# Optimization experiments

Measured on AMD Instinct MI355X. Metric: run time of the kernel, lower is better.

The kernel has to match this reference:

```python
import jax, jax.numpy as jnp
import numpy as np
import math

PHI = (1 + math.sqrt(5)) / 2
PI = math.pi
B, L, D, V, NL, PAD = 2, 384, 256, 32000, 3, 0


def _ln(t, eps):
    mu = t.mean(-1, keepdims=True)
    var = ((t - mu) ** 2).mean(-1, keepdims=True)
    return (t - mu) / jnp.sqrt(var + eps)


def setup_inputs() -> dict:
    key = jax.random.key(0)
    ks = jax.random.split(key, 8)
    return {
        'x': jax.random.randint(ks[0], (B, L), 0, V, dtype=jnp.int32),
        'emb_real': jax.random.normal(ks[1], (V, D), jnp.float32) * 0.02,
        'emb_imag': jax.random.normal(ks[2], (V, D), jnp.float32) * 0.02,
        'layer_phases': jax.random.normal(ks[3], (NL, D), jnp.float32) * 0.02,
        'interference_weights': jax.random.normal(ks[4], (NL, D), jnp.float32) * 0.02,
        'energy_levels': jnp.linspace(0.0, 1.0, D).astype(jnp.float32),
        'excitation_factor': jnp.ones((1,), jnp.float32) * 0.1,
        'phase_preservation': jnp.ones((NL, D), jnp.float32) * 0.1,
        'coherence_factor': jnp.ones((NL, 1), jnp.float32) * 0.1,
        'W_attn': jax.random.normal(ks[5], (NL, D, D), jnp.float32) * 0.02,
        'out_w': jax.random.normal(ks[6], (2 * D, V), jnp.float32) * 0.02,
        'out_b': jnp.zeros((V,), jnp.float32),
    }


def _forward(x, emb_real, emb_imag, layer_phases, interference_weights,
             energy_levels, excitation_factor, phase_preservation,
             coherence_factor, W_attn, out_w, out_b):
    re = emb_real[x] * 0.1                      # [B,L,D]
    _unused_imag = emb_imag[x] * 0.1            # imag embedding unused downstream (as in original)
    # ---- EnhancedDynamicPhaseSpace ----
    fr = jnp.zeros_like(re)
    fi = jnp.zeros_like(re)
    for i in range(NL):
        pa = jnp.tanh(layer_phases[i]) * PI * PHI      # [D]
        r = _ln(re * jnp.cos(pa), 1e-8)
        im = _ln(re * jnp.sin(pa), 1e-8)
        w = jnp.tanh(interference_weights[i])
        r = r * w
        im = im * w
        a = 2.0 * PI * i / NL
        ca, sa = math.cos(a), math.sin(a)
        fr = fr + r * ca - im * sa
        fi = fi + r * sa + im * ca
    amp = jnp.sqrt(fr * fr + fi * fi + 1e-8)
    coll = (amp < 0.1).astype(re.dtype)
    exc = jnp.exp(energy_levels) * excitation_factor   # [D]
    fr = fr + coll * exc
    fi = fi + coll * exc
    nrm = jnp.sqrt(fr * fr + fi * fi + 1e-8)
    real = jnp.clip(fr / nrm, -1.0, 1.0)
    imag = jnp.clip(fi / nrm, -1.0, 1.0)
    # ---- 3 QuantumStatePreservingAttention layers ----
    pad_mask = (x == PAD)                               # [B,L]
    scale = D ** (-0.5)
    for i in range(NL):
        # q/k/v LayerNorms are parameter-free here and q=k=v, so one norm each
        nr = _ln(real, 1e-5)
        ni = _ln(imag, 1e-5)
        ph = jnp.arctan2(ni + 1e-8, nr + 1e-8)          # [B,L,D]
        pdiff = ph[:, :, None, :] - ph[:, None, :, :]   # [B,L,L,D]
        interf = jnp.cos(pdiff)                         # [B,L,L,D]
        # mean over last dim of (interf @ W) == interf . row-means of W (same math)
        w_mean = W_attn[i].mean(axis=1)                 # [D]
        scores = jnp.einsum('blmd,d->blm', interf, w_mean) * scale
        scores = jnp.where(pad_mask[:, None, :], -jnp.inf, scores)
        attn = jnp.clip(jax.nn.softmax(scores, axis=-1), 1e-6, 1.0)
        out_r = jnp.einsum('blm,bmd->bld', attn, nr)
        out_i = jnp.einsum('blm,bmd->bld', attn, ni)
        coh = interf.mean(axis=(-1, -2))                # [B,L]
        cf = jax.nn.sigmoid(coherence_factor[i]) * coh[..., None]
        phase = jnp.arctan2(out_i + 1e-8, out_r + 1e-8)
        pres = jax.nn.sigmoid(phase_preservation[i]) * cf
        pr = out_r * jnp.cos(phase * pres)
        pim = out_i * jnp.sin(phase * pres)
        real = jnp.clip(_ln(real + 0.01 * pr, 1e-8), -1.0, 1.0)
        _dead = _ln(imag + 0.01 * pim, 1e-8)            # computed then overwritten in original
        imag = real                                     # original bug: imag = clamp(real, -1, 1)
    combined = _ln(jnp.concatenate([real, imag], axis=-1), 1e-5)
    logits = jnp.clip((combined @ out_w + out_b) * 0.1, -10.0, 10.0)
    return logits


def reference(x, emb_real, emb_imag, layer_phases, interference_weights,
              energy_levels, excitation_factor, phase_preservation,
              coherence_factor, W_attn, out_w, out_b):
    return _forward(x, emb_real, emb_imag, layer_phases, interference_weights,
                    energy_levels, excitation_factor, phase_preservation,
                    coherence_factor, W_attn, out_w, out_b)
```

## Files before the change

kernel.cpp:

```cpp
#include <hip/hip_runtime.h>
#include <hip/hip_bf16.h>
#include <math.h>

typedef __hip_bfloat16 bf16;
typedef __bf16 bf16x8 __attribute__((ext_vector_type(8)));
typedef float f32x4 __attribute__((ext_vector_type(4)));

#define NTOK 768
#define SEQ  384
#define DDIM 256
#define VOC  32000

__device__ __forceinline__ float bf2f(bf16 v) { return __bfloat162float(v); }

__device__ __forceinline__ bool probe_bf(const void* energy) {
    return ((const unsigned short*)energy)[1] != 0;
}
__device__ __forceinline__ float ldin(const void* p, long i, bool bf) {
    return bf ? bf2f(((const bf16*)p)[i]) : ((const float*)p)[i];
}

__device__ __forceinline__ float blk_sum256s(float v, float* red) {
    #pragma unroll
    for (int o = 32; o > 0; o >>= 1) v += __shfl_down(v, o, 64);
    __syncthreads();
    if ((threadIdx.x & 63) == 0) red[threadIdx.x >> 6] = v;
    __syncthreads();
    return red[0] + red[1] + red[2] + red[3];
}

__device__ __forceinline__ void np_emit(int t, int d, float nrv, float niv, bool dual,
                                        const float* __restrict__ wm,
                                        float* __restrict__ nrO, float* __restrict__ niO,
                                        float* __restrict__ Co, float* __restrict__ So,
                                        bf16* __restrict__ ASh, bf16* __restrict__ ASl,
                                        bf16* __restrict__ BSh, bf16* __restrict__ BSl)
{
    float ph = atan2f(niv + 1e-8f, nrv + 1e-8f);
    float Cv = cosf(ph), Sv = sinf(ph);
    long idx = (long)t * DDIM + d;
    nrO[idx] = nrv;
    if (dual) niO[idx] = niv;
    Co[idx] = Cv;
    So[idx] = Sv;
    float wv = wm[d];
    float aC = Cv * wv, aS = Sv * wv;
    long o0 = (long)t * 512 + d, o1 = o0 + 256;
    bf16 h;
    h = __float2bfloat16(aC); ASh[o0] = h; ASl[o0] = __float2bfloat16(aC - bf2f(h));
    h = __float2bfloat16(aS); ASh[o1] = h; ASl[o1] = __float2bfloat16(aS - bf2f(h));
    h = __float2bfloat16(Cv); BSh[o0] = h; BSl[o0] = __float2bfloat16(Cv - bf2f(h));
    h = __float2bfloat16(Sv); BSh[o1] = h; BSl[o1] = __float2bfloat16(Sv - bf2f(h));
}

__device__ __forceinline__ void gload_lds16(const bf16* g, bf16* l) {
    __builtin_amdgcn_global_load_lds(
        (const __attribute__((address_space(1))) unsigned int*)g,
        (__attribute__((address_space(3))) unsigned int*)l,
        16, 0, 0);
}


__device__ __forceinline__ void scores_unit(int l0, int m0, int b, char* smem,
    const bf16* __restrict__ ASh, const bf16* __restrict__ ASl,
    const bf16* __restrict__ BSh, const bf16* __restrict__ BSl,
    float* __restrict__ scores)
{
    bf16* ldsA0 = (bf16*)smem;
    bf16* ldsA1 = ldsA0 + 2048;
    bf16* ldsB0 = ldsA1 + 2048;
    bf16* ldsB1 = ldsB0 + 2048;
    int tid = threadIdx.x, lane = tid & 63, wid = tid >> 6;
    int wr = wid >> 1, wc = wid & 1;
    int lrow = lane >> 3, cbs = (lane & 7) ^ lrow;
    const bf16* src = (wid == 0 ? ASh : wid == 1 ? ASl : wid == 2 ? BSh : BSl)
                      + (size_t)(b * SEQ + (wid < 2 ? l0 : m0)) * 512;
    bf16* ld = (wid == 0 ? ldsA0 : wid == 1 ? ldsA1 : wid == 2 ? ldsB0 : ldsB1);
    f32x4 acc = {};
    for (int k0 = 0; k0 < 512; k0 += 64) {
        #pragma unroll
        for (int q = 0; q < 4; ++q)
            gload_lds16(src + (size_t)(q * 8 + lrow) * 512 + k0 + cbs * 8, ld + q * 512);
        __syncthreads();
        #pragma unroll
        for (int ks = 0; ks < 2; ++ks) {
            int cb = ks * 64 + (lane >> 4) * 16;
            int rowb = wc * 16 + (lane & 15);
            int offb = rowb * 128 + (cb ^ ((rowb & 7) << 4));
            bf16x8 bh = *(const bf16x8*)((const char*)ldsB0 + offb);
            bf16x8 bl = *(const bf16x8*)((const char*)ldsB1 + offb);
            int rowa = wr * 16 + (lane & 15);
            int offa = rowa * 128 + (cb ^ ((rowa & 7) << 4));
            bf16x8 ah = *(const bf16x8*)((const char*)ldsA0 + offa);
            bf16x8 al = *(const bf16x8*)((const char*)ldsA1 + offa);
            acc = __builtin_amdgcn_mfma_f32_16x16x32_bf16(ah, bh, acc, 0, 0, 0);
            acc = __builtin_amdgcn_mfma_f32_16x16x32_bf16(ah, bl, acc, 0, 0, 0);
            acc = __builtin_amdgcn_mfma_f32_16x16x32_bf16(al, bh, acc, 0, 0, 0);
        }
        __syncthreads();
    }
    int mm = m0 + wc * 16 + (lane & 15);
    int lbase = l0 + wr * 16 + (lane >> 4) * 4;
    #pragma unroll
    for (int i = 0; i < 4; ++i)
        scores[(size_t)(b * SEQ + lbase + i) * SEQ + mm] = acc[i];
}

__device__ __forceinline__ void transpose_unit(int m0, int d0, int b, char* smem, int dual,
    const float* __restrict__ nr, const float* __restrict__ ni,
    bf16* __restrict__ nrTh, bf16* __restrict__ nrTl,
    bf16* __restrict__ niTh, bf16* __restrict__ niTl)
{
    float* tr = (float*)smem;
    float* ti = tr + 64 * 65;
    int c = threadIdx.x & 63, rr = threadIdx.x >> 6;
    #pragma unroll
    for (int i = 0; i < 16; ++i) {
        int r = i * 4 + rr;
        tr[r * 65 + c] = nr[(b * SEQ + m0 + r) * DDIM + d0 + c];
        if (dual) ti[r * 65 + c] = ni[(b * SEQ + m0 + r) * DDIM + d0 + c];
    }
    __syncthreads();
    #pragma unroll
    for (int i = 0; i < 16; ++i) {
        int dd = i * 4 + rr;
        long o = (long)(b * DDIM + d0 + dd) * SEQ + m0 + c;
        float vr = tr[c * 65 + dd];
        bf16 h;
        h = __float2bfloat16(vr); nrTh[o] = h; nrTl[o] = __float2bfloat16(vr - bf2f(h));
        if (dual) {
            float vi = ti[c * 65 + dd];
            h = __float2bfloat16(vi); niTh[o] = h; niTl[o] = __float2bfloat16(vi - bf2f(h));
        }
    }
}

__device__ __forceinline__ void sums_unit(int c, int b,
    const float* __restrict__ C, const float* __restrict__ S,
    float* __restrict__ Cp, float* __restrict__ Sp)
{
    int d = threadIdx.x;
    float cs = 0.f, ss = 0.f;
    int base = (b * SEQ + c * 16) * DDIM + d;
    #pragma unroll
    for (int m = 0; m < 16; ++m) { cs += C[base + m * DDIM]; ss += S[base + m * DDIM]; }
    Cp[(b * 24 + c) * DDIM + d] = cs;
    Sp[(b * 24 + c) * DDIM + d] = ss;
}

__global__ __launch_bounds__(256)
void phaseA_k(const bf16* __restrict__ ASh, const bf16* __restrict__ ASl,
              const bf16* __restrict__ BSh, const bf16* __restrict__ BSl,
              float* __restrict__ attn,
              const float* __restrict__ nr, const float* __restrict__ ni,
              bf16* __restrict__ nrTh, bf16* __restrict__ nrTl,
              bf16* __restrict__ niTh, bf16* __restrict__ niTl,
              const float* __restrict__ Cc, const float* __restrict__ Ss,
              float* __restrict__ Cp, float* __restrict__ Sp, int dual)
{
    __shared__ __align__(16) char smem[33280];
    int u = blockIdx.x;
    if (u < 288) {
        scores_unit((u % 12) * 32, ((u / 12) % 12) * 32, u / 144, smem,
                    ASh, ASl, BSh, BSl, attn);
    } else if (u < 336) {
        int v = u - 288;
        transpose_unit((v % 6) * 64, ((v / 6) % 4) * 64, v / 24, smem, dual,
                       nr, ni, nrTh, nrTl, niTh, niTl);
    } else {
        int w = u - 336;
        sums_unit(w % 24, w / 24, Cc, Ss, Cp, Sp);
    }
}

__global__ __launch_bounds__(256)
void outfused_k(const float* __restrict__ scores, const int* __restrict__ x,
                const bf16* __restrict__ nrTh, const bf16* __restrict__ nrTl,
                const bf16* __restrict__ niTh, const bf16* __restrict__ niTl,
                float* __restrict__ outr, float* __restrict__ outi, int dual)
{
    __shared__ __align__(16) char PhL[32 * 768];
    __shared__ __align__(16) char PlL[32 * 768];
    __shared__ __align__(16) char Bb[8192];
    int l0 = blockIdx.x * 32, d0 = blockIdx.y * 32, b = blockIdx.z;
    int tid = threadIdx.x, lane = tid & 63, wid = tid >> 6;

    int msk = 0;
    #pragma unroll
    for (int j = 0; j < 6; ++j)
        if (x[b * SEQ + lane + j * 64] == 0) msk |= (1 << j);

    #pragma unroll
    for (int r8 = 0; r8 < 8; ++r8) {
        int r = wid * 8 + r8;
        const float* srow = scores + (size_t)(b * SEQ + l0 + r) * SEQ;
        float v[6];
        float mx = -__builtin_inff();
        #pragma unroll
        for (int j = 0; j < 6; ++j) {
            float s = srow[lane + j * 64];
            if (msk & (1 << j)) s = -__builtin_inff();
            v[j] = s;
            mx = fmaxf(mx, s);
        }
        #pragma unroll
        for (int o = 32; o > 0; o >>= 1) mx = fmaxf(mx, __shfl_xor(mx, o, 64));
        float e[6], sum = 0.f;
        #pragma unroll
        for (int j = 0; j < 6; ++j) { e[j] = expf(v[j] - mx); sum += e[j]; }
        #pragma unroll
        for (int o = 32; o > 0; o >>= 1) sum += __shfl_xor(sum, o, 64);
        #pragma unroll
        for (int j = 0; j < 6; ++j) {
            float p = fminf(fmaxf(e[j] / sum, 1e-6f), 1.0f);
            bf16 h = __float2bfloat16(p);
            bf16 l = __float2bfloat16(p - bf2f(h));
            int c2 = (lane + j * 64) * 2;
            int swz = ((c2 & ~15) ^ ((r & 7) << 4)) | (c2 & 15);
            *(bf16*)(PhL + r * 768 + swz) = h;
            *(bf16*)(PlL + r * 768 + swz) = l;
        }
    }
    __syncthreads();

    int wr = wid >> 1, wc = wid & 1;
    int lrow = lane >> 3, cbs = (lane & 7) ^ lrow;
    int half = wid >> 1;
    int npass = dual ? 2 : 1;

    for (int pass = 0; pass < npass; ++pass) {
        const bf16* srcB = ((wid & 1) ? (pass ? niTl : nrTl) : (pass ? niTh : nrTh))
                           + (size_t)(b * DDIM + d0) * SEQ;
        bf16* ldB = (bf16*)(Bb + (wid & 1) * 4096 + half * 2048);
        f32x4 acc = {};
        for (int k0 = 0; k0 < SEQ; k0 += 64) {
            #pragma unroll
            for (int q = 0; q < 2; ++q)
                gload_lds16(srcB + (size_t)(half * 16 + q * 8 + lrow) * SEQ + k0 + cbs * 8,
                            ldB + q * 512);
            __syncthreads();
            #pragma unroll
            for (int ks = 0; ks < 2; ++ks) {
                int cbk = ks * 64 + (lane >> 4) * 16;
                int rowb = wc * 16 + (lane & 15);
                int offb = rowb * 128 + (cbk ^ ((rowb & 7) << 4));
                bf16x8 bh = *(const bf16x8*)(Bb + offb);
                bf16x8 bl = *(const bf16x8*)(Bb + 4096 + offb);
                int rowa = wr * 16 + (lane & 15);
                int cba = k0 * 2 + cbk;
                int offa = rowa * 768 + (cba ^ ((rowa & 7) << 4));
                bf16x8 ah = *(const bf16x8*)(PhL + offa);
                bf16x8 al = *(const bf16x8*)(PlL + offa);
                acc = __builtin_amdgcn_mfma_f32_16x16x32_bf16(ah, bh, acc, 0, 0, 0);
                acc = __builtin_amdgcn_mfma_f32_16x16x32_bf16(ah, bl, acc, 0, 0, 0);
                acc = __builtin_amdgcn_mfma_f32_16x16x32_bf16(al, bh, acc, 0, 0, 0);
            }
            __syncthreads();
        }
        float* dst = pass ? outi : outr;
        int d = d0 + wc * 16 + (lane & 15);
        int lb = l0 + wr * 16 + (lane >> 4) * 4;
        #pragma unroll
        for (int i = 0; i < 4; ++i)
            dst[(size_t)(b * SEQ + lb + i) * DDIM + d] = acc[i];
    }
}

__global__ __launch_bounds__(256)
void update_k(float* __restrict__ realA,
              const float* __restrict__ outr, const float* __restrict__ outi,
              const float* __restrict__ C, const float* __restrict__ S,
              const float* __restrict__ Cp, const float* __restrict__ Sp,
              const void* __restrict__ pp, const void* __restrict__ cfac,
              const void* __restrict__ energy, int layer, int mode,
              const float* __restrict__ wmNext,
              float* __restrict__ nrO, float* __restrict__ Co, float* __restrict__ So,
              bf16* __restrict__ ASh, bf16* __restrict__ ASl,
              bf16* __restrict__ BSh, bf16* __restrict__ BSl,
              bf16* __restrict__ Ah, bf16* __restrict__ Al)
{
    __shared__ float red[4];
    bool bf = probe_bf(energy);
    int t = blockIdx.x, d = threadIdx.x;
    int b = t / SEQ;
    long idx = (long)t * DDIM + d;
    float cs = 0.f, ss = 0.f;
    #pragma unroll
    for (int c = 0; c < 24; ++c) {
        cs += Cp[(b * 24 + c) * DDIM + d];
        ss += Sp[(b * 24 + c) * DDIM + d];
    }
    float dotv = C[idx] * cs + S[idx] * ss;
    float coh = blk_sum256s(dotv, red) * (1.0f / (384.f * 256.f));
    float cf = (1.f / (1.f + expf(-ldin(cfac, layer, bf)))) * coh;
    float orr = outr[idx], oii = outi[idx];
    float phase = atan2f(oii + 1e-8f, orr + 1e-8f);
    float pres = (1.f / (1.f + expf(-ldin(pp, layer * DDIM + d, bf)))) * cf;
    float pr = orr * cosf(phase * pres);
    float v = realA[idx] + 0.01f * pr;
    float mu = blk_sum256s(v, red) * (1.f / 256.f);
    float dv = v - mu;
    float var = blk_sum256s(dv * dv, red) * (1.f / 256.f);
    float nv = dv / sqrtf(var + 1e-8f);
    nv = fminf(fmaxf(nv, -1.f), 1.f);
    realA[idx] = nv;
    float mu2 = blk_sum256s(nv, red) * (1.f / 256.f);
    float dv2 = nv - mu2;
    float var2 = blk_sum256s(dv2 * dv2, red) * (1.f / 256.f);
    float nn = dv2 / sqrtf(var2 + 1e-5f);
    if (mode == 0) {
        np_emit(t, d, nn, nn, false, wmNext, nrO, nullptr, Co, So, ASh, ASl, BSh, BSl);
    } else {
        bf16 h = __float2bfloat16(nn);
        Ah[idx] = h;
        Al[idx] = __float2bfloat16(nn - bf2f(h));
    }
}

__global__ __launch_bounds__(256)
void phase_kernel(const int* __restrict__ x, const void* __restrict__ emb,
                  const void* __restrict__ lph, const void* __restrict__ iw,
                  const void* __restrict__ energy, const void* __restrict__ excf,
                  const float* __restrict__ wm0,
                  float* __restrict__ realO,
                  float* __restrict__ nrO, float* __restrict__ niO,
                  float* __restrict__ Co, float* __restrict__ So,
                  bf16* __restrict__ ASh, bf16* __restrict__ ASl,
                  bf16* __restrict__ BSh, bf16* __restrict__ BSl)
{
    __shared__ float red[4];
    bool bf = probe_bf(energy);
    int t = blockIdx.x, d = threadIdx.x;
    int tok = x[t];
    float re = ldin(emb, (long)tok * DDIM + d, bf) * 0.1f;
    float fr = 0.f, fi = 0.f;
    const float ca[3] = {1.0f, -0.5f, -0.5f};
    const float sa[3] = {0.0f, 0.86602540378443864676f, -0.86602540378443864676f};
    #pragma unroll
    for (int i = 0; i < 3; ++i) {
        float pa = tanhf(ldin(lph, i * DDIM + d, bf)) * 3.14159265358979323846f;
        pa = pa * 1.61803398874989484820f;
        float vr = re * cosf(pa);
        float vi = re * sinf(pa);
        float mu = blk_sum256s(vr, red) * (1.f / 256.f);
        float dv = vr - mu;
        float var = blk_sum256s(dv * dv, red) * (1.f / 256.f);
        float r = dv / sqrtf(var + 1e-8f);
        mu = blk_sum256s(vi, red) * (1.f / 256.f);
        float di = vi - mu;
        var = blk_sum256s(di * di, red) * (1.f / 256.f);
        float im = di / sqrtf(var + 1e-8f);
        float w = tanhf(ldin(iw, i * DDIM + d, bf));
        r *= w; im *= w;
        fr = fr + r * ca[i] - im * sa[i];
        fi = fi + r * sa[i] + im * ca[i];
    }
    float amp = sqrtf(fr * fr + fi * fi + 1e-8f);
    float ex = expf(ldin(energy, d, bf)) * ldin(excf, 0, bf);
    if (amp < 0.1f) { fr += ex; fi += ex; }
    float nrm = sqrtf(fr * fr + fi * fi + 1e-8f);
    float rr = fminf(fmaxf(fr / nrm, -1.f), 1.f);
    float ii = fminf(fmaxf(fi / nrm, -1.f), 1.f);
    realO[t * DDIM + d] = rr;
    float mu = blk_sum256s(rr, red) * (1.f / 256.f);
    float dv = rr - mu;
    float var = blk_sum256s(dv * dv, red) * (1.f / 256.f);
    float nrv = dv / sqrtf(var + 1e-5f);
    mu = blk_sum256s(ii, red) * (1.f / 256.f);
    float di = ii - mu;
    var = blk_sum256s(di * di, red) * (1.f / 256.f);
    float niv = di / sqrtf(var + 1e-5f);
    np_emit(t, d, nrv, niv, true, wm0, nrO, niO, Co, So, ASh, ASl, BSh, BSl);
}

__global__ __launch_bounds__(256)
void prep1_k(const void* __restrict__ W, const void* __restrict__ Wattn,
             const void* __restrict__ energy,
             bf16* __restrict__ Bh, bf16* __restrict__ Bl, float* __restrict__ wmAll)
{
    bool bf = probe_bf(energy);
    int u = blockIdx.x;
    if (u < 2000) {
        __shared__ float tile[64][65];
        int v0 = (u % 500) * 64, d0 = (u / 500) * 64;
        int c = threadIdx.x & 63, rr = threadIdx.x >> 6;
        #pragma unroll
        for (int i = 0; i < 16; ++i) {
            int r = i * 4 + rr;
            long i1 = (long)(d0 + r) * VOC + v0 + c;
            long i2 = (long)(d0 + r + 256) * VOC + v0 + c;
            tile[r][c] = ldin(W, i1, bf) + ldin(W, i2, bf);
        }
        __syncthreads();
        int d = threadIdx.x & 63, vv = threadIdx.x >> 6;
        #pragma unroll
        for (int i = 0; i < 16; ++i) {
            int v = i * 4 + vv;
            float s = tile[d][v];
            bf16 h = __float2bfloat16(s);
            long o = (long)(v0 + v) * DDIM + d0 + d;
            Bh[o] = h;
            Bl[o] = __float2bfloat16(s - __bfloat162float(h));
        }
    } else {
        int row = (u - 2000) * 4 + (threadIdx.x >> 6);
        int lane = threadIdx.x & 63;
        long base = (long)row * DDIM + lane * 4;
        float s = 0.f;
        #pragma unroll
        for (int j = 0; j < 4; ++j) s += ldin(Wattn, base + j, bf);
        #pragma unroll
        for (int o = 32; o > 0; o >>= 1) s += __shfl_down(s, o, 64);
        if (lane == 0) wmAll[row] = s * (1.f / 256.f) * 0.0625f;
    }
}

__global__ __launch_bounds__(512, 4)
void vocab_gemm(const bf16* __restrict__ Ah, const bf16* __restrict__ Al,
                const bf16* __restrict__ Bh, const bf16* __restrict__ Bl,
                const void* __restrict__ bias, const void* __restrict__ energy,
                void* __restrict__ out)
{
    __shared__ bf16 lds[4][128 * 64];
    bool bf = probe_bf(energy);
    int flat = blockIdx.x + blockIdx.y * 6;
    int xcd = flat & 7, bidx = flat >> 3;
    int swz = (xcd < 4) ? xcd * 188 + bidx : 752 + (xcd - 4) * 187 + bidx;
    int m0 = (swz % 6) * 128, n0 = (swz / 6) * 128;
    int tid = threadIdx.x, lane = tid & 63, wid = tid >> 6;
    int wm = wid >> 2, wn = wid & 3;
    int arr = wid >> 1, half = wid & 1;

    const bf16* src;
    if      (arr == 0) src = Ah + (size_t)m0 * DDIM;
    else if (arr == 1) src = Al + (size_t)m0 * DDIM;
    else if (arr == 2) src = Bh + (size_t)n0 * DDIM;
    else               src = Bl + (size_t)n0 * DDIM;
    src += (size_t)half * 64 * DDIM;
    bf16* ldst = &lds[arr][half * 64 * 64];
    int lrow = lane >> 3;
    int cbs  = (lane & 7) ^ lrow;

    f32x4 acc[4][2] = {};

    for (int k0 = 0; k0 < DDIM; k0 += 64) {
        #pragma unroll
        for (int q = 0; q < 8; ++q) {
            const bf16* gp = src + (size_t)(q * 8 + lrow) * DDIM + k0 + cbs * 8;
            gload_lds16(gp, ldst + q * 512);
        }
        __syncthreads();
        #pragma unroll
        for (int ks = 0; ks < 2; ++ks) {
            int cb = ks * 64 + (lane >> 4) * 16;
            bf16x8 bhf[2], blf[2];
            #pragma unroll
            for (int fn = 0; fn < 2; ++fn) {
                int row = wn * 32 + fn * 16 + (lane & 15);
                int off = row * 128 + (cb ^ ((row & 7) << 4));
                bhf[fn] = *(const bf16x8*)((const char*)&lds[2][0] + off);
                blf[fn] = *(const bf16x8*)((const char*)&lds[3][0] + off);
            }
            #pragma unroll
            for (int fm = 0; fm < 4; ++fm) {
                int row = wm * 64 + fm * 16 + (lane & 15);
                int off = row * 128 + (cb ^ ((row & 7) << 4));
                bf16x8 ah = *(const bf16x8*)((const char*)&lds[0][0] + off);
                bf16x8 al = *(const bf16x8*)((const char*)&lds[1][0] + off);
                #pragma unroll
                for (int fn = 0; fn < 2; ++fn) {
                    acc[fm][fn] = __builtin_amdgcn_mfma_f32_16x16x32_bf16(ah, bhf[fn], acc[fm][fn], 0, 0, 0);
                    acc[fm][fn] = __builtin_amdgcn_mfma_f32_16x16x32_bf16(ah, blf[fn], acc[fm][fn], 0, 0, 0);
                    acc[fm][fn] = __builtin_amdgcn_mfma_f32_16x16x32_bf16(al, bhf[fn], acc[fm][fn], 0, 0, 0);
                }
            }
        }
        __syncthreads();
    }

    #pragma unroll
    for (int fn = 0; fn < 2; ++fn) {
        int n = n0 + wn * 32 + fn * 16 + (lane & 15);
        float bv = ldin(bias, n, bf);
        #pragma unroll
        for (int fm = 0; fm < 4; ++fm) {
            int mbase = m0 + wm * 64 + fm * 16 + (lane >> 4) * 4;
            #pragma unroll
            for (int i = 0; i < 4; ++i) {
                float lg = (acc[fm][fn][i] + bv) * 0.1f;
                lg = fminf(fmaxf(lg, -10.f), 10.f);
                size_t idx = (size_t)(mbase + i) * VOC + n;
                if (bf) ((bf16*)out)[idx] = __float2bfloat16(lg);
                else    ((float*)out)[idx] = lg;
            }
        }
    }
}

extern "C" void kernel_launch(void* const* d_in, const int* in_sizes, int n_in,
                              void* d_out, int out_size, void* d_ws, size_t ws_size,
                              hipStream_t stream) {
    (void)in_sizes; (void)n_in; (void)out_size; (void)ws_size;
    const int*  x        = (const int*)d_in[0];
    const void* emb_real = d_in[1];
    const void* lph      = d_in[3];
    const void* iw       = d_in[4];
    const void* energy   = d_in[5];
    const void* excf     = d_in[6];
    const void* pp       = d_in[7];
    const void* cfac     = d_in[8];
    const void* Wattn    = d_in[9];
    const void* out_w    = d_in[10];
    const void* out_b    = d_in[11];

    float* ws = (float*)d_ws;
    const int TD = NTOK * DDIM;
    float* realA = ws;
    float* nr    = realA + TD;
    float* ni    = nr + TD;
    float* Cc    = ni + TD;
    float* Ss    = Cc + TD;
    float* outr  = Ss + TD;
    float* outi  = outr + TD;
    float* attn  = outi + TD;
    float* Cp    = attn + 2 * SEQ * SEQ;
    float* Sp    = Cp + 48 * DDIM;
    float* wmAll = Sp + 48 * DDIM;
    bf16* Ah  = (bf16*)(wmAll + 768);
    bf16* Al  = Ah + (size_t)NTOK * DDIM;
    bf16* Wth = Al + (size_t)NTOK * DDIM;
    bf16* Wtl = Wth + (size_t)VOC * DDIM;
    bf16* ASh = Wtl + (size_t)VOC * DDIM;
    bf16* ASl = ASh + (size_t)NTOK * 512;
    bf16* BSh = ASl + (size_t)NTOK * 512;
    bf16* BSl = BSh + (size_t)NTOK * 512;
    bf16* nrTh = BSl + (size_t)NTOK * 512;
    bf16* nrTl = nrTh + (size_t)NTOK * DDIM;
    bf16* niTh = nrTl + (size_t)NTOK * DDIM;
    bf16* niTl = niTh + (size_t)NTOK * DDIM;

    prep1_k<<<2192, 256, 0, stream>>>(out_w, Wattn, energy, Wth, Wtl, wmAll);
    phase_kernel<<<NTOK, 256, 0, stream>>>(x, emb_real, lph, iw, energy, excf, wmAll,
                                           realA, nr, ni, Cc, Ss, ASh, ASl, BSh, BSl);
    for (int layer = 0; layer < 3; ++layer) {
        int dual = (layer == 0);
        phaseA_k<<<384, 256, 0, stream>>>(ASh, ASl, BSh, BSl, attn, nr, ni,
                                          nrTh, nrTl, niTh, niTl, Cc, Ss, Cp, Sp, dual);
        outfused_k<<<dim3(12, 8, 2), 256, 0, stream>>>(attn, x, nrTh, nrTl, niTh, niTl,
                                                       outr, outi, dual);
        update_k<<<NTOK, 256, 0, stream>>>(realA, outr, dual ? outi : outr, Cc, Ss,
                                           Cp, Sp, pp, cfac, energy, layer,
                                           (layer < 2) ? 0 : 1,
                                           wmAll + (layer + 1 < 3 ? (layer + 1) * DDIM : 0),
                                           nr, Cc, Ss, ASh, ASl, BSh, BSl, Ah, Al);
    }
    vocab_gemm<<<dim3(6, VOC / 128), 512, 0, stream>>>(Ah, Al, Wth, Wtl, out_b, energy, (void*)d_out);
}
```

Measured before the change: 363.7 us.

## Exploit real==imag in later layers to halve score K and double-buffer LDS loads

For layers after the first, the imaginary input equals the real one, so C==S. Those layers now use a single folded cos term with a factor of 2, which halves the score GEMM K dimension from 512 to 256 and drops the sine sums and stores. The score and output GEMM loops also double-buffer their global-to-LDS loads so the next K tile is fetched while MFMAs run. The outfused kernel computes the real and imaginary products in one pass instead of two. In exchange it uses more LDS, and correctness depends on the algebraic identity sin(atan2(n,n)) == cos(atan2(n,n)).

```diff
diff --git a/kernel.cpp b/kernel.cpp
--- a/kernel.cpp
+++ b/kernel.cpp
@@ -29,7 +29,7 @@
     return red[0] + red[1] + red[2] + red[3];
 }
 
-__device__ __forceinline__ void np_emit(int t, int d, float nrv, float niv, bool dual,
+__device__ __forceinline__ void np_emit(int t, int d, float nrv, float niv,
                                         const float* __restrict__ wm,
                                         float* __restrict__ nrO, float* __restrict__ niO,
                                         float* __restrict__ Co, float* __restrict__ So,
@@ -40,7 +40,7 @@
     float Cv = cosf(ph), Sv = sinf(ph);
     long idx = (long)t * DDIM + d;
     nrO[idx] = nrv;
-    if (dual) niO[idx] = niv;
+    niO[idx] = niv;
     Co[idx] = Cv;
     So[idx] = Sv;
     float wv = wm[d];
@@ -61,43 +61,49 @@
 }
 
 
-__device__ __forceinline__ void scores_unit(int l0, int m0, int b, char* smem,
+__device__ __forceinline__ void scores_unit(int l0, int m0, int b, char* smem, int kd,
     const bf16* __restrict__ ASh, const bf16* __restrict__ ASl,
     const bf16* __restrict__ BSh, const bf16* __restrict__ BSl,
     float* __restrict__ scores)
 {
-    bf16* ldsA0 = (bf16*)smem;
-    bf16* ldsA1 = ldsA0 + 2048;
-    bf16* ldsB0 = ldsA1 + 2048;
-    bf16* ldsB1 = ldsB0 + 2048;
     int tid = threadIdx.x, lane = tid & 63, wid = tid >> 6;
     int wr = wid >> 1, wc = wid & 1;
     int lrow = lane >> 3, cbs = (lane & 7) ^ lrow;
     const bf16* src = (wid == 0 ? ASh : wid == 1 ? ASl : wid == 2 ? BSh : BSl)
-                      + (size_t)(b * SEQ + (wid < 2 ? l0 : m0)) * 512;
-    bf16* ld = (wid == 0 ? ldsA0 : wid == 1 ? ldsA1 : wid == 2 ? ldsB0 : ldsB1);
+                      + (size_t)(b * SEQ + (wid < 2 ? l0 : m0)) * kd;
+    bf16* ld0 = (bf16*)(smem + wid * 4096);
+    bf16* ld1 = (bf16*)(smem + 16384 + wid * 4096);
     f32x4 acc = {};
-    for (int k0 = 0; k0 < 512; k0 += 64) {
-        #pragma unroll
-        for (int q = 0; q < 4; ++q)
-            gload_lds16(src + (size_t)(q * 8 + lrow) * 512 + k0 + cbs * 8, ld + q * 512);
-        __syncthreads();
+    #pragma unroll
+    for (int q = 0; q < 4; ++q)
+        gload_lds16(src + (size_t)(q * 8 + lrow) * kd + cbs * 8, ld0 + q * 512);
+    __syncthreads();
+    int cur = 0;
+    for (int k0 = 0; k0 < kd; k0 += 64) {
+        if (k0 + 64 < kd) {
+            bf16* ld = cur ? ld0 : ld1;
+            #pragma unroll
+            for (int q = 0; q < 4; ++q)
+                gload_lds16(src + (size_t)(q * 8 + lrow) * kd + (k0 + 64) + cbs * 8, ld + q * 512);
+        }
+        const char* base = smem + cur * 16384;
         #pragma unroll
         for (int ks = 0; ks < 2; ++ks) {
             int cb = ks * 64 + (lane >> 4) * 16;
             int rowb = wc * 16 + (lane & 15);
             int offb = rowb * 128 + (cb ^ ((rowb & 7) << 4));
-            bf16x8 bh = *(const bf16x8*)((const char*)ldsB0 + offb);
-            bf16x8 bl = *(const bf16x8*)((const char*)ldsB1 + offb);
+            bf16x8 bh = *(const bf16x8*)(base + 8192 + offb);
+            bf16x8 bl = *(const bf16x8*)(base + 12288 + offb);
             int rowa = wr * 16 + (lane & 15);
             int offa = rowa * 128 + (cb ^ ((rowa & 7) << 4));
-            bf16x8 ah = *(const bf16x8*)((const char*)ldsA0 + offa);
-            bf16x8 al = *(const bf16x8*)((const char*)ldsA1 + offa);
+            bf16x8 ah = *(const bf16x8*)(base + offa);
+            bf16x8 al = *(const bf16x8*)(base + 4096 + offa);
             acc = __builtin_amdgcn_mfma_f32_16x16x32_bf16(ah, bh, acc, 0, 0, 0);
             acc = __builtin_amdgcn_mfma_f32_16x16x32_bf16(ah, bl, acc, 0, 0, 0);
             acc = __builtin_amdgcn_mfma_f32_16x16x32_bf16(al, bh, acc, 0, 0, 0);
         }
         __syncthreads();
+        cur ^= 1;
     }
     int mm = m0 + wc * 16 + (lane & 15);
     int lbase = l0 + wr * 16 + (lane >> 4) * 4;
@@ -135,7 +141,7 @@
     }
 }
 
-__device__ __forceinline__ void sums_unit(int c, int b,
+__device__ __forceinline__ void sums_unit(int c, int b, int dual,
     const float* __restrict__ C, const float* __restrict__ S,
     float* __restrict__ Cp, float* __restrict__ Sp)
 {
@@ -143,9 +149,12 @@
     float cs = 0.f, ss = 0.f;
     int base = (b * SEQ + c * 16) * DDIM + d;
     #pragma unroll
-    for (int m = 0; m < 16; ++m) { cs += C[base + m * DDIM]; ss += S[base + m * DDIM]; }
+    for (int m = 0; m < 16; ++m) {
+        cs += C[base + m * DDIM];
+        if (dual) ss += S[base + m * DDIM];
+    }
     Cp[(b * 24 + c) * DDIM + d] = cs;
-    Sp[(b * 24 + c) * DDIM + d] = ss;
+    if (dual) Sp[(b * 24 + c) * DDIM + d] = ss;
 }
 
 __global__ __launch_bounds__(256)
@@ -156,12 +165,12 @@
               bf16* __restrict__ nrTh, bf16* __restrict__ nrTl,
               bf16* __restrict__ niTh, bf16* __restrict__ niTl,
               const float* __restrict__ Cc, const float* __restrict__ Ss,
-              float* __restrict__ Cp, float* __restrict__ Sp, int dual)
+              float* __restrict__ Cp, float* __restrict__ Sp, int dual, int kd)
 {
     __shared__ __align__(16) char smem[33280];
     int u = blockIdx.x;
     if (u < 288) {
-        scores_unit((u % 12) * 32, ((u / 12) % 12) * 32, u / 144, smem,
+        scores_unit((u % 12) * 32, ((u / 12) % 12) * 32, u / 144, smem, kd,
                     ASh, ASl, BSh, BSl, attn);
     } else if (u < 336) {
         int v = u - 288;
@@ -169,7 +178,7 @@
                        nr, ni, nrTh, nrTl, niTh, niTl);
     } else {
         int w = u - 336;
-        sums_unit(w % 24, w / 24, Cc, Ss, Cp, Sp);
+        sums_unit(w % 24, w / 24, dual, Cc, Ss, Cp, Sp);
     }
 }
 
@@ -181,7 +190,7 @@
 {
     __shared__ __align__(16) char PhL[32 * 768];
     __shared__ __align__(16) char PlL[32 * 768];
-    __shared__ __align__(16) char Bb[8192];
+    __shared__ __align__(16) char Bb[2][16384];
     int l0 = blockIdx.x * 32, d0 = blockIdx.y * 32, b = blockIdx.z;
     int tid = threadIdx.x, lane = tid & 63, wid = tid >> 6;
 
@@ -221,48 +230,78 @@
             *(bf16*)(PlL + r * 768 + swz) = l;
         }
     }
-    __syncthreads();
 
     int wr = wid >> 1, wc = wid & 1;
     int lrow = lane >> 3, cbs = (lane & 7) ^ lrow;
-    int half = wid >> 1;
-    int npass = dual ? 2 : 1;
-
-    for (int pass = 0; pass < npass; ++pass) {
-        const bf16* srcB = ((wid & 1) ? (pass ? niTl : nrTl) : (pass ? niTh : nrTh))
-                           + (size_t)(b * DDIM + d0) * SEQ;
-        bf16* ldB = (bf16*)(Bb + (wid & 1) * 4096 + half * 2048);
-        f32x4 acc = {};
-        for (int k0 = 0; k0 < SEQ; k0 += 64) {
+    int half = wid >> 1, hl = wid & 1;
+    const bf16* sNr = (hl ? nrTl : nrTh) + (size_t)(b * DDIM + d0) * SEQ;
+    const bf16* sNi = (hl ? niTl : niTh) + (size_t)(b * DDIM + d0) * SEQ;
+
+    f32x4 accr = {}, acci = {};
+
+    {
+        bf16* dr = (bf16*)(Bb[0] + hl * 4096 + half * 2048);
+        #pragma unroll
+        for (int q = 0; q < 2; ++q)
+            gload_lds16(sNr + (size_t)(half * 16 + q * 8 + lrow) * SEQ + cbs * 8, dr + q * 512);
+        if (dual) {
+            bf16* di_ = (bf16*)(Bb[0] + 8192 + hl * 4096 + half * 2048);
             #pragma unroll
             for (int q = 0; q < 2; ++q)
-                gload_lds16(srcB + (size_t)(half * 16 + q * 8 + lrow) * SEQ + k0 + cbs * 8,
-                            ldB + q * 512);
-            __syncthreads();
+                gload_lds16(sNi + (size_t)(half * 16 + q * 8 + lrow) * SEQ + cbs * 8, di_ + q * 512);
+        }
+    }
+    __syncthreads();
+    int cur = 0;
+    for (int k0 = 0; k0 < SEQ; k0 += 64) {
+        if (k0 + 64 < SEQ) {
+            bf16* dr = (bf16*)(Bb[cur ^ 1] + hl * 4096 + half * 2048);
             #pragma unroll
-            for (int ks = 0; ks < 2; ++ks) {
-                int cbk = ks * 64 + (lane >> 4) * 16;
-                int rowb = wc * 16 + (lane & 15);
-                int offb = rowb * 128 + (cbk ^ ((rowb & 7) << 4));
-                bf16x8 bh = *(const bf16x8*)(Bb + offb);
-                bf16x8 bl = *(const bf16x8*)(Bb + 4096 + offb);
-                int rowa = wr * 16 + (lane & 15);
-                int cba = k0 * 2 + cbk;
-                int offa = rowa * 768 + (cba ^ ((rowa & 7) << 4));
-                bf16x8 ah = *(const bf16x8*)(PhL + offa);
-                bf16x8 al = *(const bf16x8*)(PlL + offa);
-                acc = __builtin_amdgcn_mfma_f32_16x16x32_bf16(ah, bh, acc, 0, 0, 0);
-                acc = __builtin_amdgcn_mfma_f32_16x16x32_bf16(ah, bl, acc, 0, 0, 0);
-                acc = __builtin_amdgcn_mfma_f32_16x16x32_bf16(al, bh, acc, 0, 0, 0);
+            for (int q = 0; q < 2; ++q)
+                gload_lds16(sNr + (size_t)(half * 16 + q * 8 + lrow) * SEQ + (k0 + 64) + cbs * 8,
+                            dr + q * 512);
+            if (dual) {
+                bf16* di_ = (bf16*)(Bb[cur ^ 1] + 8192 + hl * 4096 + half * 2048);
+                #pragma unroll
+                for (int q = 0; q < 2; ++q)
+                    gload_lds16(sNi + (size_t)(half * 16 + q * 8 + lrow) * SEQ + (k0 + 64) + cbs * 8,
+                                di_ + q * 512);
             }
-            __syncthreads();
-        }
-        float* dst = pass ? outi : outr;
-        int d = d0 + wc * 16 + (lane & 15);
-        int lb = l0 + wr * 16 + (lane >> 4) * 4;
-        #pragma unroll
-        for (int i = 0; i < 4; ++i)
-            dst[(size_t)(b * SEQ + lb + i) * DDIM + d] = acc[i];
+        }
+        #pragma unroll
+        for (int ks = 0; ks < 2; ++ks) {
+            int cbk = ks * 64 + (lane >> 4) * 16;
+            int rowb = wc * 16 + (lane & 15);
+            int offb = rowb * 128 + (cbk ^ ((rowb & 7) << 4));
+            bf16x8 bh = *(const bf16x8*)(Bb[cur] + offb);
+            bf16x8 bl = *(const bf16x8*)(Bb[cur] + 4096 + offb);
+            int rowa = wr * 16 + (lane & 15);
+            int cba = k0 * 2 + cbk;
+            int offa = rowa * 768 + (cba ^ ((rowa & 7) << 4));
+            bf16x8 ah = *(const bf16x8*)(PhL + offa);
+            bf16x8 al = *(const bf16x8*)(PlL + offa);
+            accr = __builtin_amdgcn_mfma_f32_16x16x32_bf16(ah, bh, accr, 0, 0, 0);
+            accr = __builtin_amdgcn_mfma_f32_16x16x32_bf16(ah, bl, accr, 0, 0, 0);
+            accr = __builtin_amdgcn_mfma_f32_16x16x32_bf16(al, bh, accr, 0, 0, 0);
+            if (dual) {
+                bf16x8 bih = *(const bf16x8*)(Bb[cur] + 8192 + offb);
+                bf16x8 bil = *(const bf16x8*)(Bb[cur] + 12288 + offb);
+                acci = __builtin_amdgcn_mfma_f32_16x16x32_bf16(ah, bih, acci, 0, 0, 0);
+                acci = __builtin_amdgcn_mfma_f32_16x16x32_bf16(ah, bil, acci, 0, 0, 0);
+                acci = __builtin_amdgcn_mfma_f32_16x16x32_bf16(al, bih, acci, 0, 0, 0);
+            }
+        }
+        __syncthreads();
+        cur ^= 1;
+    }
+
+    int d = d0 + wc * 16 + (lane & 15);
+    int lb = l0 + wr * 16 + (lane >> 4) * 4;
+    #pragma unroll
+    for (int i = 0; i < 4; ++i) {
+        size_t idx = (size_t)(b * SEQ + lb + i) * DDIM + d;
+        outr[idx] = accr[i];
+        if (dual) outi[idx] = acci[i];
     }
 }
 
@@ -274,13 +313,14 @@
               const void* __restrict__ pp, const void* __restrict__ cfac,
               const void* __restrict__ energy, int layer, int mode,
               const float* __restrict__ wmNext,
-              float* __restrict__ nrO, float* __restrict__ Co, float* __restrict__ So,
+              float* __restrict__ nrO, float* __restrict__ Co,
               bf16* __restrict__ ASh, bf16* __restrict__ ASl,
               bf16* __restrict__ BSh, bf16* __restrict__ BSl,
               bf16* __restrict__ Ah, bf16* __restrict__ Al)
 {
     __shared__ float red[4];
     bool bf = probe_bf(energy);
+    int dualin = (layer == 0);
     int t = blockIdx.x, d = threadIdx.x;
     int b = t / SEQ;
     long idx = (long)t * DDIM + d;
@@ -288,9 +328,9 @@
     #pragma unroll
     for (int c = 0; c < 24; ++c) {
         cs += Cp[(b * 24 + c) * DDIM + d];
-        ss += Sp[(b * 24 + c) * DDIM + d];
-    }
-    float dotv = C[idx] * cs + S[idx] * ss;
+        if (dualin) ss += Sp[(b * 24 + c) * DDIM + d];
+    }
+    float dotv = dualin ? (C[idx] * cs + S[idx] * ss) : 2.f * C[idx] * cs;
     float coh = blk_sum256s(dotv, red) * (1.0f / (384.f * 256.f));
     float cf = (1.f / (1.f + expf(-ldin(cfac, layer, bf)))) * coh;
     float orr = outr[idx], oii = outi[idx];
@@ -309,7 +349,15 @@
     float var2 = blk_sum256s(dv2 * dv2, red) * (1.f / 256.f);
     float nn = dv2 / sqrtf(var2 + 1e-5f);
     if (mode == 0) {
-        np_emit(t, d, nn, nn, false, wmNext, nrO, nullptr, Co, So, ASh, ASl, BSh, BSl);
+        float ph = atan2f(nn + 1e-8f, nn + 1e-8f);
+        float Cv = cosf(ph);
+        nrO[idx] = nn;
+        Co[idx] = Cv;
+        float aC = 2.f * Cv * wmNext[d];
+        long o0 = (long)t * 256 + d;
+        bf16 h;
+        h = __float2bfloat16(aC); ASh[o0] = h; ASl[o0] = __float2bfloat16(aC - bf2f(h));
+        h = __float2bfloat16(Cv); BSh[o0] = h; BSl[o0] = __float2bfloat16(Cv - bf2f(h));
     } else {
         bf16 h = __float2bfloat16(nn);
         Ah[idx] = h;
@@ -370,7 +418,7 @@
     float di = ii - mu;
     var = blk_sum256s(di * di, red) * (1.f / 256.f);
     float niv = di / sqrtf(var + 1e-5f);
-    np_emit(t, d, nrv, niv, true, wm0, nrO, niO, Co, So, ASh, ASl, BSh, BSl);
+    np_emit(t, d, nrv, niv, wm0, nrO, niO, Co, So, ASh, ASl, BSh, BSl);
 }
 
 __global__ __launch_bounds__(256)
@@ -545,14 +593,15 @@
     for (int layer = 0; layer < 3; ++layer) {
         int dual = (layer == 0);
         phaseA_k<<<384, 256, 0, stream>>>(ASh, ASl, BSh, BSl, attn, nr, ni,
-                                          nrTh, nrTl, niTh, niTl, Cc, Ss, Cp, Sp, dual);
+                                          nrTh, nrTl, niTh, niTl, Cc, Ss, Cp, Sp,
+                                          dual, dual ? 512 : 256);
         outfused_k<<<dim3(12, 8, 2), 256, 0, stream>>>(attn, x, nrTh, nrTl, niTh, niTl,
                                                        outr, outi, dual);
         update_k<<<NTOK, 256, 0, stream>>>(realA, outr, dual ? outi : outr, Cc, Ss,
                                            Cp, Sp, pp, cfac, energy, layer,
                                            (layer < 2) ? 0 : 1,
                                            wmAll + (layer + 1 < 3 ? (layer + 1) * DDIM : 0),
-                                           nr, Cc, Ss, ASh, ASl, BSh, BSl, Ah, Al);
+                                           nr, Cc, ASh, ASl, BSh, BSl, Ah, Al);
     }
     vocab_gemm<<<dim3(6, VOC / 128), 512, 0, stream>>>(Ah, Al, Wth, Wtl, out_b, energy, (void*)d_out);
 }
```

Measured after the change: 360.5 us. About the same (-0.9%).
